# Optimization experiments

Hardware: AMD Instinct MI355X
Metric: run time of the kernel (lower is better)

## Reference

```python
import jax, jax.numpy as jnp
import numpy as np

G = 512            # voxel grid extent per axis
B = 2              # batches
N_PER_BATCH = 20000
EPS = 1e-5
SLOPE = 0.01       # LeakyReLU default negative_slope
OFFS = [(dx, dy, dz) for dx in (-1, 0, 1) for dy in (-1, 0, 1) for dz in (-1, 0, 1)]


def _keys(coords, stride):
    # coords: [N,4] int32 (batch,x,y,z), multiples of stride -> unique int32 key
    Gs = G // stride
    c = coords[:, 1:] // stride
    return ((coords[:, 0] * Gs + c[:, 0]) * Gs + c[:, 1]) * Gs + c[:, 2]


def _sorted_keys(in_coords, in_stride):
    keys = _keys(in_coords, in_stride)
    perm = jnp.argsort(keys)
    return keys[perm], perm


def _query(ks, perm, out_coords, off, in_stride):
    # hash-free kernel-map lookup: binary search of neighbor key in sorted keys
    q = out_coords[:, 1:] + jnp.array(off, jnp.int32) * in_stride
    valid = jnp.all((q >= 0) & (q < G), axis=1)
    qc = jnp.clip(q, 0, G - 1) // in_stride
    Gs = G // in_stride
    qk = ((out_coords[:, 0] * Gs + qc[:, 0]) * Gs + qc[:, 1]) * Gs + qc[:, 2]
    pos = jnp.clip(jnp.searchsorted(ks, qk), 0, ks.shape[0] - 1)
    hit = valid & (ks[pos] == qk)
    return jnp.where(hit, perm[pos], 0), hit


def sparse_conv(feats, in_coords, out_coords, W, in_stride):
    # gather-GEMM-scatter sparse conv, kernel 3^3, W: [27, Cin, Cout]
    ks, perm = _sorted_keys(in_coords, in_stride)
    out = jnp.zeros((out_coords.shape[0], W.shape[-1]), feats.dtype)
    for k, off in enumerate(OFFS):
        idx, hit = _query(ks, perm, out_coords, off, in_stride)
        f = jnp.where(hit[:, None], feats[idx], jnp.zeros((), feats.dtype))
        out = out + f @ W[k]
    return out


def sparse_maxpool(feats, in_coords, out_coords, in_stride):
    ks, perm = _sorted_keys(in_coords, in_stride)
    NEG = jnp.asarray(-3.0e38, feats.dtype)
    out = jnp.full((out_coords.shape[0], feats.shape[1]), NEG, feats.dtype)
    for off in OFFS:
        idx, hit = _query(ks, perm, out_coords, off, in_stride)
        out = jnp.maximum(out, jnp.where(hit[:, None], feats[idx], NEG))
    return out


def slice_to_field(level_feats, level_coords, field_coords, stride):
    # TensorField.slice: map coarse sparse features back to every field point
    ks, perm = _sorted_keys(level_coords, stride)
    qk = _keys(field_coords, stride)
    pos = jnp.clip(jnp.searchsorted(ks, qk), 0, ks.shape[0] - 1)
    return level_feats[perm[pos]]


def bn_lrelu(x, gamma, beta):
    # MinkowskiBatchNorm (training-mode batch stats) + LeakyReLU
    mu = x.mean(0)
    var = ((x - mu) ** 2).mean(0)
    y = (x - mu) * jax.lax.rsqrt(var + EPS) * gamma + beta
    return jnp.where(y >= 0, y, SLOPE * y)


def setup_inputs() -> dict:
    rng = np.random.default_rng(0)
    coords_np = []
    for b in range(B):
        lin = np.unique(rng.integers(0, G ** 3, size=2 * N_PER_BATCH, dtype=np.int64))
        rng.shuffle(lin)
        lin = lin[:N_PER_BATCH]
        x, r = lin // (G * G), lin % (G * G)
        coords_np.append(np.stack([np.full(N_PER_BATCH, b, np.int64), x, r // G, r % G], 1))
    coords_np = np.concatenate(coords_np, 0)

    def level(s):
        q = coords_np.copy()
        q[:, 1:] = (q[:, 1:] // s) * s
        key = ((q[:, 0] * G + q[:, 1]) * G + q[:, 2]) * G + q[:, 3]
        uk = np.unique(key)
        b, r = uk // G ** 3, uk % G ** 3
        return np.stack([b, r // (G * G), (r // G) % G, r % G], 1).astype(np.int32)

    levels = {('c%d' % s): jnp.asarray(level(s)) for s in (2, 4, 8, 16, 32, 64, 128)}
    ks = jax.random.split(jax.random.key(0), 9)

    def conv_w(k, cin, cout):
        return jax.random.normal(k, (27, cin, cout), jnp.float32) * np.float32(np.sqrt(2.0 / (27 * cin)))

    inp = dict(
        feats=jax.random.normal(ks[0], (coords_np.shape[0], 1), jnp.float32),
        coords=jnp.asarray(coords_np.astype(np.int32)),
        w_mlp=jax.random.normal(ks[1], (1, 32), jnp.float32),
        gm=jnp.ones(32, jnp.float32), bm=jnp.zeros(32, jnp.float32),
        W1=conv_w(ks[2], 32, 48), g1=jnp.ones(48, jnp.float32), b1=jnp.zeros(48, jnp.float32),
        W2=conv_w(ks[3], 48, 64), g2=jnp.ones(64, jnp.float32), b2=jnp.zeros(64, jnp.float32),
        W3=conv_w(ks[4], 64, 96), g3=jnp.ones(96, jnp.float32), b3=jnp.zeros(96, jnp.float32),
        W4=conv_w(ks[5], 96, 128), g4=jnp.ones(128, jnp.float32), b4=jnp.zeros(128, jnp.float32),
        W5a=conv_w(ks[6], 336, 256), g5a=jnp.ones(256, jnp.float32), b5a=jnp.zeros(256, jnp.float32),
        W5b=conv_w(ks[7], 256, 512), g5b=jnp.ones(512, jnp.float32), b5b=jnp.zeros(512, jnp.float32),
        W5c=conv_w(ks[8], 512, 1024), g5c=jnp.ones(1024, jnp.float32), b5c=jnp.zeros(1024, jnp.float32),
    )
    inp.update(levels)
    return inp


def reference(feats, coords, c2, c4, c8, c16, c32, c64, c128, w_mlp, gm, bm,
              W1, g1, b1, W2, g2, b2, W3, g3, b3, W4, g4, b4,
              W5a, g5a, b5a, W5b, g5b, b5b, W5c, g5c, b5c):
    # mlp1 on the tensor field (coords are unique, so field == sparse tensor)
    x = bn_lrelu(feats @ w_mlp, gm, bm)                            # [N,32]
    y = bn_lrelu(sparse_conv(x, coords, coords, W1, 1), g1, b1)    # stride 1, 48
    y1 = sparse_maxpool(y, coords, c2, 1)                          # stride 2
    y = bn_lrelu(sparse_conv(y1, c2, c4, W2, 2), g2, b2)           # stride 4, 64
    y2 = sparse_maxpool(y, c4, c8, 4)                              # stride 8
    y = bn_lrelu(sparse_conv(y2, c8, c16, W3, 8), g3, b3)          # stride 16, 96
    y3 = sparse_maxpool(y, c16, c32, 16)                           # stride 32
    y = bn_lrelu(sparse_conv(y3, c32, c64, W4, 32), g4, b4)        # stride 64, 128
    y4 = sparse_maxpool(y, c64, c128, 64)                          # stride 128
    x1 = slice_to_field(y1, c2, coords, 2)
    x2 = slice_to_field(y2, c8, coords, 8)
    x3 = slice_to_field(y3, c32, coords, 32)
    x4 = slice_to_field(y4, c128, coords, 128)
    xc = jnp.concatenate([x1, x2, x3, x4], axis=1)                 # [N,336]
    y = bn_lrelu(sparse_conv(xc, coords, c2, W5a, 1), g5a, b5a)    # stride 2, 256
    y = bn_lrelu(sparse_conv(y, c2, c4, W5b, 2), g5b, b5b)         # stride 4, 512
    y = bn_lrelu(sparse_conv(y, c4, c8, W5c, 4), g5c, b5c)         # stride 8, 1024
    return y
```

## Files before the change

kernel.cpp:

```cpp
#include <hip/hip_runtime.h>
#include <cstdint>
#include <cstddef>

#define GDIM 512

typedef __attribute__((ext_vector_type(8))) short short8;
typedef __attribute__((ext_vector_type(4))) float f32x4;
typedef __attribute__((ext_vector_type(4))) unsigned short ushort4v;

__device__ __forceinline__ short f2bf(float f) {
  unsigned u = __float_as_uint(f);
  u = u + 0x7fffu + ((u >> 16) & 1u);
  return (short)(u >> 16);
}

__device__ __forceinline__ int hash_lookup(int key, const int* __restrict__ keys,
                                           const int* __restrict__ vals, unsigned capmask) {
  unsigned slot = ((unsigned)key * 2654435761u) & capmask;
  while (true) {
    int kk = keys[slot];
    if (kk == key) return vals[slot];
    if (kk == -1) return -1;
    slot = (slot + 1) & capmask;
  }
}

__global__ void k_build_table(const int* __restrict__ coords, int n, int sh, int Gs,
                              int* __restrict__ keys, int* __restrict__ vals, unsigned capmask) {
  int i = blockIdx.x * blockDim.x + threadIdx.x;
  if (i >= n) return;
  int b = coords[4 * i];
  int key = ((b * Gs + (coords[4 * i + 1] >> sh)) * Gs + (coords[4 * i + 2] >> sh)) * Gs +
            (coords[4 * i + 3] >> sh);
  unsigned slot = ((unsigned)key * 2654435761u) & capmask;
  while (true) {
    int prev = atomicCAS(&keys[slot], -1, key);
    if (prev == -1) { vals[slot] = i; return; }
    slot = (slot + 1) & capmask;
  }
}

__global__ void k_query_idx_t(const int* __restrict__ oc, int m, int sh, int Gs,
                              const int* __restrict__ keys, const int* __restrict__ vals,
                              unsigned capmask, int* __restrict__ idxT) {
  int k = blockIdx.y;
  int o = blockIdx.x * blockDim.x + threadIdx.x;
  if (o >= m) return;
  int stride = 1 << sh;
  int dx = k / 9 - 1, dy = (k / 3) % 3 - 1, dz = k % 3 - 1;
  int4 c = *(const int4*)(oc + 4 * o);
  int qx = c.y + dx * stride;
  int qy = c.z + dy * stride;
  int qz = c.w + dz * stride;
  int res = -1;
  if ((unsigned)qx < GDIM && (unsigned)qy < GDIM && (unsigned)qz < GDIM) {
    int key = ((c.x * Gs + (qx >> sh)) * Gs + (qy >> sh)) * Gs + (qz >> sh);
    res = hash_lookup(key, keys, vals, capmask);
  }
  idxT[(size_t)k * m + o] = res;
}

__global__ void k_make_pairs(const int* __restrict__ idxT, int m,
                             int* __restrict__ po_o, int* __restrict__ pi_o,
                             int* __restrict__ po_r, int* __restrict__ pi_r,
                             int* __restrict__ cnts, int mcap) {
  int o = blockIdx.x * blockDim.x + threadIdx.x;
  bool act = o < m;
  int lane = threadIdx.x & 63;
  bool owned = false;
  for (int k = 0; k < 27; ++k) {
    int i = act ? idxT[(size_t)k * m + o] : -1;
    bool hit = i >= 0;
    bool isown = hit && !owned;
    if (isown) owned = true;
    bool isrest = hit && !isown;
    unsigned long long bo = __ballot(isown);
    if (bo) {
      int ldr = __ffsll((unsigned long long)bo) - 1;
      int base = 0;
      if (lane == ldr) base = atomicAdd(&cnts[k], __popcll(bo));
      base = __shfl(base, ldr);
      if (isown) {
        int p = base + __popcll(bo & ((1ull << lane) - 1ull));
        po_o[k * mcap + p] = o;
        pi_o[k * mcap + p] = i;
      }
    }
    unsigned long long br = __ballot(isrest);
    if (br) {
      int ldr = __ffsll((unsigned long long)br) - 1;
      int base = 0;
      if (lane == ldr) base = atomicAdd(&cnts[27 + k], __popcll(br));
      base = __shfl(base, ldr);
      if (isrest) {
        int p = base + __popcll(br & ((1ull << lane) - 1ull));
        po_r[k * mcap + p] = o;
        pi_r[k * mcap + p] = i;
      }
    }
  }
}

template<bool OWNER>
__global__ __launch_bounds__(256) void k_conv_mfma(
    const unsigned short* __restrict__ Fb,
    const short* __restrict__ Wt,
    float* __restrict__ out,
    const int* __restrict__ plo, const int* __restrict__ pli,
    const int* __restrict__ counts, int cin, int cin_pad, int cout, int mcap) {
  int k = blockIdx.z;
  int cnt = counts[k];
  int p0 = blockIdx.x * 64;
  if (p0 >= cnt) return;
  int np = min(64, cnt - p0);

  __shared__ short Alds[64 * 136];
  __shared__ short Blds[2][128 * 40];
  __shared__ int rows_out[64];
  __shared__ int rows_in[64];

  int tid = threadIdx.x;
  if (tid < 64) {
    rows_out[tid] = (tid < np) ? plo[k * mcap + p0 + tid] : -1;
    rows_in [tid] = (tid < np) ? pli[k * mcap + p0 + tid] : -1;
  }

  int wave = tid >> 6, lane = tid & 63;
  int wm = (wave & 1) * 32, wn = (wave >> 1) * 64;
  int lm = lane & 15, quad = lane >> 4;
  const short* Wk = Wt + (size_t)k * cout * cin;
  int nT = (cout + 127) >> 7;
  int nSlab = (cin_pad + 127) >> 7;

  int bn0 = (tid) >> 2, bk0 = (tid & 3) << 3;
  int bn1 = (tid + 256) >> 2, bk1 = ((tid + 256) & 3) << 3;

  for (int nt0 = 0; nt0 < nT; ++nt0) {
    int n0 = nt0 << 7;
    f32x4 acc[2][4] = {};
    for (int ks = 0; ks < cin_pad; ks += 128) {
      int kslab = min(128, cin_pad - ks);
      int aStride = kslab + 8;
      __syncthreads();
      if (nSlab > 1 || nt0 == 0) {
        int clog = kslab == 128 ? 4 : (kslab == 64 ? 3 : 2);
        for (int u = tid; u < (64 << clog); u += 256) {
          int r = u >> clog;
          int kc = (u - (r << clog)) << 3;
          int gk = ks + kc;
          int irow = rows_in[r];
          short8 v = {0, 0, 0, 0, 0, 0, 0, 0};
          if (irow >= 0 && gk < cin)
            v = *(const short8*)((const short*)Fb + (size_t)irow * cin + gk);
          *(short8*)(Alds + r * aStride + kc) = v;
        }
      }
      int nsl = kslab >> 5;
      short8 br0 = {0, 0, 0, 0, 0, 0, 0, 0}, br1 = br0;
      {
        int gn = n0 + bn0, gk = ks + bk0;
        if (gn < cout && gk < cin) br0 = *(const short8*)(Wk + (size_t)gn * cin + gk);
        gn = n0 + bn1; gk = ks + bk1;
        if (gn < cout && gk < cin) br1 = *(const short8*)(Wk + (size_t)gn * cin + gk);
      }
      for (int j = 0; j < nsl; ++j) {
        __syncthreads();
        *(short8*)(&Blds[j & 1][bn0 * 40 + bk0]) = br0;
        *(short8*)(&Blds[j & 1][bn1 * 40 + bk1]) = br1;
        if (j + 1 < nsl) {
          int gkbase = ks + (j + 1) * 32;
          short8 z = {0, 0, 0, 0, 0, 0, 0, 0};
          br0 = z; br1 = z;
          int gn = n0 + bn0, gk = gkbase + bk0;
          if (gn < cout && gk < cin) br0 = *(const short8*)(Wk + (size_t)gn * cin + gk);
          gn = n0 + bn1; gk = gkbase + bk1;
          if (gn < cout && gk < cin) br1 = *(const short8*)(Wk + (size_t)gn * cin + gk);
        }
        __syncthreads();
        int ka = j * 32 + quad * 8;
        short8 a0 = *(const short8*)(Alds + (wm + lm) * aStride + ka);
        short8 a1 = *(const short8*)(Alds + (wm + 16 + lm) * aStride + ka);
        #pragma unroll
        for (int nt = 0; nt < 4; ++nt) {
          short8 b = *(const short8*)(&Blds[j & 1][(wn + nt * 16 + lm) * 40 + quad * 8]);
          acc[0][nt] = __builtin_amdgcn_mfma_f32_16x16x32_bf16(a0, b, acc[0][nt], 0, 0, 0);
          acc[1][nt] = __builtin_amdgcn_mfma_f32_16x16x32_bf16(a1, b, acc[1][nt], 0, 0, 0);
        }
      }
    }
    #pragma unroll
    for (int mt = 0; mt < 2; ++mt)
      #pragma unroll
      for (int nt = 0; nt < 4; ++nt)
        #pragma unroll
        for (int r = 0; r < 4; ++r) {
          int row = wm + mt * 16 + quad * 4 + r;
          int col = n0 + wn + nt * 16 + lm;
          if (row < np && col < cout) {
            if (OWNER)
              out[(size_t)rows_out[row] * cout + col] = acc[mt][nt][r];
            else
              atomicAdd(&out[(size_t)rows_out[row] * cout + col], acc[mt][nt][r]);
          }
        }
  }
}

__global__ void k_convert_w(const float* __restrict__ W, short* __restrict__ Wt,
                            int cin, int cout) {
  __shared__ float tile[32][33];
  int k = blockIdx.z;
  int n0 = blockIdx.x * 32, c0 = blockIdx.y * 32;
  int tx = threadIdx.x & 31, ty = threadIdx.x >> 5;
  const float* Wk = W + (size_t)k * cin * cout;
  for (int i = ty; i < 32; i += 8) {
    int c = c0 + i, n = n0 + tx;
    tile[i][tx] = (c < cin && n < cout) ? Wk[(size_t)c * cout + n] : 0.f;
  }
  __syncthreads();
  short* Wtk = Wt + (size_t)k * cout * cin;
  for (int i = ty; i < 32; i += 8) {
    int n = n0 + i, c = c0 + tx;
    if (n < cout && c < cin) Wtk[(size_t)n * cin + c] = f2bf(tile[tx][i]);
  }
}

__global__ void k_query_idx(const int* __restrict__ oc, int m, int sh, int Gs,
                            const int* __restrict__ keys, const int* __restrict__ vals,
                            unsigned capmask, int* __restrict__ idx) {
  int t = blockIdx.x * blockDim.x + threadIdx.x;
  if (t >= m * 27) return;
  int o = t / 27, k = t - o * 27;
  int stride = 1 << sh;
  int dx = k / 9 - 1, dy = (k / 3) % 3 - 1, dz = k % 3 - 1;
  int b  = oc[4 * o];
  int qx = oc[4 * o + 1] + dx * stride;
  int qy = oc[4 * o + 2] + dy * stride;
  int qz = oc[4 * o + 3] + dz * stride;
  int res = -1;
  if ((unsigned)qx < GDIM && (unsigned)qy < GDIM && (unsigned)qz < GDIM) {
    int key = ((b * Gs + (qx >> sh)) * Gs + (qy >> sh)) * Gs + (qz >> sh);
    res = hash_lookup(key, keys, vals, capmask);
  }
  idx[t] = res;
}

__global__ void k_maxpool_bn(const float* __restrict__ F, unsigned short* __restrict__ out,
                             const int* __restrict__ idx, int m, int C,
                             const float* __restrict__ ab) {
  long long t = (long long)blockIdx.x * blockDim.x + threadIdx.x;
  if (t >= (long long)m * C) return;
  int o = (int)(t / C), c = (int)(t - (long long)o * C);
  float a = ab[c], b = ab[C + c];
  float best = -3e38f;
  #pragma unroll 1
  for (int k = 0; k < 27; ++k) {
    int i = idx[o * 27 + k];
    if (i >= 0) {
      float y = a * F[(size_t)i * C + c] + b;
      y = fmaxf(y, 0.01f * y);
      best = fmaxf(best, y);
    }
  }
  out[t] = (unsigned short)f2bf(best);
}

__global__ void k_slice_idx(const int* __restrict__ coords, int n, int sh, int Gs,
                            const int* __restrict__ keys, const int* __restrict__ vals,
                            unsigned capmask, int* __restrict__ sidx) {
  int i = blockIdx.x * blockDim.x + threadIdx.x;
  if (i >= n) return;
  int b = coords[4 * i];
  int key = ((b * Gs + (coords[4 * i + 1] >> sh)) * Gs + (coords[4 * i + 2] >> sh)) * Gs +
            (coords[4 * i + 3] >> sh);
  int v = hash_lookup(key, keys, vals, capmask);
  sidx[i] = (v < 0) ? 0 : v;
}

__global__ void k_gather_cols16(const unsigned short* __restrict__ src, int C,
                                const int* __restrict__ sidx,
                                unsigned short* __restrict__ dst, int dstC, int colOff, int n) {
  long long t = (long long)blockIdx.x * blockDim.x + threadIdx.x;
  if (t >= (long long)n * C) return;
  int o = (int)(t / C), c = (int)(t - (long long)o * C);
  dst[(size_t)o * dstC + colOff + c] = src[(size_t)sidx[o] * C + c];
}

__global__ void k_mlp(const float* __restrict__ feats, const float* __restrict__ w,
                      float* __restrict__ x, int n) {
  int t = blockIdx.x * blockDim.x + threadIdx.x;
  if (t >= n * 32) return;
  x[t] = feats[t >> 5] * w[t & 31];
}

__global__ void k_bn_stats(const float* __restrict__ x, int m, int C,
                           float* __restrict__ sums) {
  __shared__ float ls[2][256];
  int tid = threadIdx.x;
  int RL = (C >= 256) ? 1 : (256 / C);
  int c, rl;
  bool active;
  if (C >= 256) { c = blockIdx.y * 256 + tid; rl = 0; active = true; }
  else { c = tid % C; rl = tid / C; active = (tid < RL * C); }
  float s = 0.f, s2 = 0.f;
  if (active) {
    int step = gridDim.x * RL;
    for (int r = blockIdx.x * RL + rl; r < m; r += step) {
      float v = x[(size_t)r * C + c];
      s += v; s2 += v * v;
    }
  }
  if (RL == 1) {
    atomicAdd(&sums[c], s);
    atomicAdd(&sums[C + c], s2);
  } else {
    ls[0][tid] = s; ls[1][tid] = s2;
    __syncthreads();
    if (tid < C) {
      for (int j = 1; j < RL; ++j) { s += ls[0][c + j * C]; s2 += ls[1][c + j * C]; }
      atomicAdd(&sums[c], s);
      atomicAdd(&sums[C + c], s2);
    }
  }
}

__global__ void k_bn_finalize(const float* __restrict__ sums, const float* __restrict__ gamma,
                              const float* __restrict__ beta, int C, float inv_m,
                              float* __restrict__ ab) {
  for (int c = threadIdx.x; c < C; c += 256) {
    float mu  = sums[c] * inv_m;
    float var = sums[C + c] * inv_m - mu * mu;
    float a = rsqrtf(var + 1e-5f) * gamma[c];
    ab[c] = a;
    ab[C + c] = beta[c] - mu * a;
  }
}

__global__ void k_bn_bf16(const float* __restrict__ x, unsigned short* __restrict__ xb,
                          long long total4, int C, const float* __restrict__ ab) {
  long long t = (long long)blockIdx.x * blockDim.x + threadIdx.x;
  if (t >= total4) return;
  long long e = t * 4;
  int c = (int)(e % C);
  float4 v = *(const float4*)(x + e);
  ushort4v o;
  float y0 = ab[c] * v.x + ab[C + c];         o.x = (unsigned short)f2bf(fmaxf(y0, 0.01f * y0));
  float y1 = ab[c + 1] * v.y + ab[C + c + 1]; o.y = (unsigned short)f2bf(fmaxf(y1, 0.01f * y1));
  float y2 = ab[c + 2] * v.z + ab[C + c + 2]; o.z = (unsigned short)f2bf(fmaxf(y2, 0.01f * y2));
  float y3 = ab[c + 3] * v.w + ab[C + c + 3]; o.w = (unsigned short)f2bf(fmaxf(y3, 0.01f * y3));
  *(ushort4v*)(xb + e) = o;
}

__global__ void k_bn_apply(float* __restrict__ x, long long total4, int C,
                           const float* __restrict__ ab) {
  long long t = (long long)blockIdx.x * blockDim.x + threadIdx.x;
  if (t >= total4) return;
  long long e = t * 4;
  int c = (int)(e % C);
  float4 v = *(const float4*)(x + e);
  float y0 = ab[c] * v.x + ab[C + c];         v.x = fmaxf(y0, 0.01f * y0);
  float y1 = ab[c + 1] * v.y + ab[C + c + 1]; v.y = fmaxf(y1, 0.01f * y1);
  float y2 = ab[c + 2] * v.z + ab[C + c + 2]; v.z = fmaxf(y2, 0.01f * y2);
  float y3 = ab[c + 3] * v.w + ab[C + c + 3]; v.w = fmaxf(y3, 0.01f * y3);
  *(float4*)(x + e) = v;
}

static inline int cdiv(int a, int b) { return (a + b - 1) / b; }

extern "C" void kernel_launch(void* const* d_in, const int* in_sizes, int n_in,
                              void* d_out, int out_size, void* d_ws, size_t ws_size,
                              hipStream_t stream) {
  (void)n_in; (void)out_size; (void)ws_size;
  const float* feats  = (const float*)d_in[0];
  const int*   coords = (const int*)d_in[1];
  const float* w_mlp = (const float*)d_in[2];
  const float* gm  = (const float*)d_in[3];  const float* bm  = (const float*)d_in[4];
  const float* W1  = (const float*)d_in[5];  const float* g1  = (const float*)d_in[6];  const float* b1  = (const float*)d_in[7];
  const float* W2  = (const float*)d_in[8];  const float* g2  = (const float*)d_in[9];  const float* b2  = (const float*)d_in[10];
  const float* W3  = (const float*)d_in[11]; const float* g3  = (const float*)d_in[12]; const float* b3  = (const float*)d_in[13];
  const float* W4  = (const float*)d_in[14]; const float* g4  = (const float*)d_in[15]; const float* b4  = (const float*)d_in[16];
  const float* W5a = (const float*)d_in[17]; const float* g5a = (const float*)d_in[18]; const float* b5a = (const float*)d_in[19];
  const float* W5b = (const float*)d_in[20]; const float* g5b = (const float*)d_in[21]; const float* b5b = (const float*)d_in[22];
  const float* W5c = (const float*)d_in[23]; const float* g5c = (const float*)d_in[24]; const float* b5c = (const float*)d_in[25];
  const int*   lvl[7];
  for (int i = 0; i < 7; ++i) lvl[i] = (const int*)d_in[26 + i];

  const int N = in_sizes[0];
  int nl[7];
  for (int i = 0; i < 7; ++i) nl[i] = in_sizes[26 + i] / 4;
  const int n2 = nl[0], n4 = nl[1], n8 = nl[2], n16 = nl[3], n32 = nl[4], n64 = nl[5], n128 = nl[6];

  char* ws = (char*)d_ws;
  size_t off = 0;
  auto alloc = [&](size_t bytes) -> char* {
    off = (off + 255) & ~(size_t)255;
    char* p = ws + off;
    off += bytes;
    return p;
  };

  struct Tab { int* keys; int* vals; unsigned mask; int sh; int Gs; int n; const int* src; };
  Tab tab[8];
  const int* tsrc[8] = {coords, lvl[0], lvl[1], lvl[2], lvl[3], lvl[4], lvl[5], lvl[6]};
  int tn[8] = {N, n2, n4, n8, n16, n32, n64, n128};
  for (int i = 0; i < 8; ++i) {
    int cap = 64;
    while (cap < 2 * tn[i]) cap <<= 1;
    tab[i].keys = (int*)alloc((size_t)cap * 4);
    tab[i].vals = (int*)alloc((size_t)cap * 4);
    tab[i].mask = (unsigned)(cap - 1);
    tab[i].sh = i;
    tab[i].Gs = GDIM >> i;
    tab[i].n = tn[i];
    tab[i].src = tsrc[i];
  }

  int* pout   = (int*)alloc((size_t)27 * N * 4);
  int* pin    = (int*)alloc((size_t)27 * N * 4);
  int* pout_r = (int*)alloc((size_t)27 * N * 4);
  int* pin_r  = (int*)alloc((size_t)27 * N * 4);
  int* counts = (int*)alloc(256);
  int* idxbuf = (int*)alloc((size_t)27 * N * 4);
  int* sidx[4];
  for (int i = 0; i < 4; ++i) sidx[i] = (int*)alloc((size_t)N * 4);
  float* bnsum = (float*)alloc(2 * 1024 * 4);
  float* abuf  = (float*)alloc(2 * 1024 * 4);

  auto mxz = [](size_t a, size_t b) { return a > b ? a : b; };
  size_t szA = mxz(mxz((size_t)N * 32, (size_t)n4 * 64), (size_t)n64 * 128) * 4;
  size_t szB = mxz(mxz((size_t)N * 48, (size_t)n16 * 96), (size_t)n2 * 256) * 4;
  float* RA = (float*)alloc(szA);
  float* RB = (float*)alloc(szB);
  float* RG = (float*)alloc((size_t)n4 * 512 * 4);
  unsigned short* xb  = (unsigned short*)alloc((size_t)N * 32 * 2);
  unsigned short* y1b = (unsigned short*)alloc((size_t)n2 * 48 * 2);
  unsigned short* y2b = (unsigned short*)alloc((size_t)n8 * 64 * 2);
  unsigned short* y3b = (unsigned short*)alloc((size_t)n32 * 96 * 2);
  unsigned short* y4b = (unsigned short*)alloc((size_t)n128 * 128 * 2);
  unsigned short* xcb = (unsigned short*)alloc((size_t)N * 336 * 2);
  unsigned short* t5bb = (unsigned short*)alloc((size_t)n4 * 512 * 2);
  short* Wt1  = (short*)alloc((size_t)27 * 32 * 48 * 2);
  short* Wt2  = (short*)alloc((size_t)27 * 48 * 64 * 2);
  short* Wt3  = (short*)alloc((size_t)27 * 64 * 96 * 2);
  short* Wt4  = (short*)alloc((size_t)27 * 96 * 128 * 2);
  short* Wt5a = (short*)alloc((size_t)27 * 336 * 256 * 2);
  short* Wt5b = (short*)alloc((size_t)27 * 256 * 512 * 2);
  short* Wt5c = (short*)alloc((size_t)27 * 512 * 1024 * 2);

  for (int i = 0; i < 8; ++i)
    hipMemsetAsync(tab[i].keys, 0xFF, (size_t)(tab[i].mask + 1) * 4, stream);
  for (int i = 0; i < 8; ++i)
    k_build_table<<<cdiv(tab[i].n, 256), 256, 0, stream>>>(
        tab[i].src, tab[i].n, tab[i].sh, tab[i].Gs, tab[i].keys, tab[i].vals, tab[i].mask);

  auto convW = [&](const float* W, short* Wt, int cin, int cout) {
    dim3 g(cdiv(cout, 32), cdiv(cin, 32), 27);
    k_convert_w<<<g, 256, 0, stream>>>(W, Wt, cin, cout);
  };
  convW(W1, Wt1, 32, 48);     convW(W2, Wt2, 48, 64);
  convW(W3, Wt3, 64, 96);     convW(W4, Wt4, 96, 128);
  convW(W5a, Wt5a, 336, 256); convW(W5b, Wt5b, 256, 512);
  convW(W5c, Wt5c, 512, 1024);

  auto conv = [&](const unsigned short* Fb, const short* Wt, const int* oc, int m,
                  const Tab& t, int cin, int cout, float* out) {
    hipMemsetAsync(counts, 0, 54 * 4, stream);
    dim3 gq(cdiv(m, 256), 27);
    k_query_idx_t<<<gq, 256, 0, stream>>>(oc, m, t.sh, t.Gs, t.keys, t.vals, t.mask, idxbuf);
    k_make_pairs<<<cdiv(m, 256), 256, 0, stream>>>(idxbuf, m, pout, pin, pout_r, pin_r,
                                                   counts, N);
    int cin_pad = cin <= 32 ? 32 : (cin <= 64 ? 64 : ((cin + 127) & ~127));
    dim3 grid(cdiv(m, 64), 1, 27);
    k_conv_mfma<true><<<grid, 256, 0, stream>>>(Fb, Wt, out, pout, pin, counts,
                                                cin, cin_pad, cout, N);
    k_conv_mfma<false><<<grid, 256, 0, stream>>>(Fb, Wt, out, pout_r, pin_r, counts + 27,
                                                 cin, cin_pad, cout, N);
  };
  auto stats = [&](const float* x, int m, int C, const float* gamma, const float* beta) {
    hipMemsetAsync(bnsum, 0, (size_t)2 * C * 4, stream);
    int CG = (C >= 256) ? (C / 256) : 1;
    int RL = (C >= 256) ? 1 : (256 / C);
    int NS = (C >= 256) ? 512 : 256;
    int maxNS = cdiv(m, RL);
    if (NS > maxNS) NS = maxNS < 1 ? 1 : maxNS;
    dim3 g(NS, CG);
    k_bn_stats<<<g, 256, 0, stream>>>(x, m, C, bnsum);
    k_bn_finalize<<<1, 256, 0, stream>>>(bnsum, gamma, beta, C, 1.0f / (float)m, abuf);
  };
  auto pool = [&](const float* F, const int* oc, int m, const Tab& t, int C,
                  unsigned short* out) {
    k_query_idx<<<cdiv(m * 27, 256), 256, 0, stream>>>(
        oc, m, t.sh, t.Gs, t.keys, t.vals, t.mask, idxbuf);
    long long total = (long long)m * C;
    k_maxpool_bn<<<(int)((total + 255) / 256), 256, 0, stream>>>(F, out, idxbuf, m, C, abuf);
  };
  auto cvt = [&](const float* src, unsigned short* dst, long long total, int C) {
    long long t4 = total / 4;
    k_bn_bf16<<<(int)((t4 + 255) / 256), 256, 0, stream>>>(src, dst, t4, C, abuf);
  };

  float* x = RA;
  k_mlp<<<cdiv(N * 32, 256), 256, 0, stream>>>(feats, w_mlp, x, N);
  stats(x, N, 32, gm, bm);
  cvt(x, xb, (long long)N * 32, 32);

  float* t1 = RB;
  conv(xb, Wt1, coords, N, tab[0], 32, 48, t1);
  stats(t1, N, 48, g1, b1);
  pool(t1, lvl[0], n2, tab[0], 48, y1b);

  float* t2 = RA;
  conv(y1b, Wt2, lvl[1], n4, tab[1], 48, 64, t2);
  stats(t2, n4, 64, g2, b2);
  pool(t2, lvl[2], n8, tab[2], 64, y2b);

  float* t3 = RB;
  conv(y2b, Wt3, lvl[3], n16, tab[3], 64, 96, t3);
  stats(t3, n16, 96, g3, b3);
  pool(t3, lvl[4], n32, tab[4], 96, y3b);

  float* t4 = RA;
  conv(y3b, Wt4, lvl[5], n64, tab[5], 96, 128, t4);
  stats(t4, n64, 128, g4, b4);
  pool(t4, lvl[6], n128, tab[6], 128, y4b);

  k_slice_idx<<<cdiv(N, 256), 256, 0, stream>>>(coords, N, tab[1].sh, tab[1].Gs,
                                                tab[1].keys, tab[1].vals, tab[1].mask, sidx[0]);
  k_slice_idx<<<cdiv(N, 256), 256, 0, stream>>>(coords, N, tab[3].sh, tab[3].Gs,
                                                tab[3].keys, tab[3].vals, tab[3].mask, sidx[1]);
  k_slice_idx<<<cdiv(N, 256), 256, 0, stream>>>(coords, N, tab[5].sh, tab[5].Gs,
                                                tab[5].keys, tab[5].vals, tab[5].mask, sidx[2]);
  k_slice_idx<<<cdiv(N, 256), 256, 0, stream>>>(coords, N, tab[7].sh, tab[7].Gs,
                                                tab[7].keys, tab[7].vals, tab[7].mask, sidx[3]);
  k_gather_cols16<<<(int)(((long long)N * 48 + 255) / 256), 256, 0, stream>>>(y1b, 48, sidx[0], xcb, 336, 0, N);
  k_gather_cols16<<<(int)(((long long)N * 64 + 255) / 256), 256, 0, stream>>>(y2b, 64, sidx[1], xcb, 336, 48, N);
  k_gather_cols16<<<(int)(((long long)N * 96 + 255) / 256), 256, 0, stream>>>(y3b, 96, sidx[2], xcb, 336, 112, N);
  k_gather_cols16<<<(int)(((long long)N * 128 + 255) / 256), 256, 0, stream>>>(y4b, 128, sidx[3], xcb, 336, 208, N);

  float* t5a = RB;
  conv(xcb, Wt5a, lvl[0], n2, tab[0], 336, 256, t5a);
  stats(t5a, n2, 256, g5a, b5a);
  unsigned short* t5ab = xcb;
  cvt(t5a, t5ab, (long long)n2 * 256, 256);

  float* t5b = RG;
  conv(t5ab, Wt5b, lvl[1], n4, tab[1], 256, 512, t5b);
  stats(t5b, n4, 512, g5b, b5b);
  cvt(t5b, t5bb, (long long)n4 * 512, 512);

  float* outp = (float*)d_out;
  conv(t5bb, Wt5c, lvl[2], n8, tab[2], 512, 1024, outp);
  stats(outp, n8, 1024, g5c, b5c);
  long long total4 = (long long)n8 * 1024 / 4;
  k_bn_apply<<<(int)((total4 + 255) / 256), 256, 0, stream>>>(outp, total4, 1024, abuf);
}
```

Baseline: 1.960 ms.

## Compact conv grid via per-offset block plan and split output tiles across grid

Adds a tiny planning kernel that prefix-sums the per-offset pair counts into block offsets. The conv kernel then uses a persistent, grid-stride loop over only the non-empty 64-pair tiles instead of launching cdiv(m,64)*27 blocks, most of which exit immediately. Output-column tiles move from an inner loop onto grid.y, which adds parallelism but means the gathered A tile is reloaded once per output tile. It also adds one extra launch and a serial scan per conv.

```diff
diff --git a/kernel.cpp b/kernel.cpp
--- a/kernel.cpp
+++ b/kernel.cpp
@@ -101,59 +101,73 @@
   }
 }
 
+__global__ void k_plan(const int* __restrict__ cnts, int* __restrict__ plan) {
+  if (threadIdx.x == 0) {
+    int acc = 0;
+    for (int k = 0; k < 27; ++k) { plan[k] = acc; acc += (cnts[k] + 63) >> 6; }
+    plan[27] = acc;
+    acc = 0;
+    for (int k = 0; k < 27; ++k) { plan[28 + k] = acc; acc += (cnts[27 + k] + 63) >> 6; }
+    plan[55] = acc;
+  }
+}
+
 template<bool OWNER>
 __global__ __launch_bounds__(256) void k_conv_mfma(
     const unsigned short* __restrict__ Fb,
     const short* __restrict__ Wt,
     float* __restrict__ out,
     const int* __restrict__ plo, const int* __restrict__ pli,
-    const int* __restrict__ counts, int cin, int cin_pad, int cout, int mcap) {
-  int k = blockIdx.z;
-  int cnt = counts[k];
-  int p0 = blockIdx.x * 64;
-  if (p0 >= cnt) return;
-  int np = min(64, cnt - p0);
-
+    const int* __restrict__ counts, const int* __restrict__ plan,
+    int cin, int cin_pad, int cout, int mcap) {
+  __shared__ int pshared[28];
   __shared__ short Alds[64 * 136];
   __shared__ short Blds[2][128 * 40];
   __shared__ int rows_out[64];
   __shared__ int rows_in[64];
 
   int tid = threadIdx.x;
-  if (tid < 64) {
-    rows_out[tid] = (tid < np) ? plo[k * mcap + p0 + tid] : -1;
-    rows_in [tid] = (tid < np) ? pli[k * mcap + p0 + tid] : -1;
-  }
-
+  if (tid < 28) pshared[tid] = plan[tid];
+  __syncthreads();
+  int NB = pshared[27];
+
+  int n0 = blockIdx.y << 7;
   int wave = tid >> 6, lane = tid & 63;
   int wm = (wave & 1) * 32, wn = (wave >> 1) * 64;
   int lm = lane & 15, quad = lane >> 4;
-  const short* Wk = Wt + (size_t)k * cout * cin;
-  int nT = (cout + 127) >> 7;
-  int nSlab = (cin_pad + 127) >> 7;
-
   int bn0 = (tid) >> 2, bk0 = (tid & 3) << 3;
   int bn1 = (tid + 256) >> 2, bk1 = ((tid + 256) & 3) << 3;
 
-  for (int nt0 = 0; nt0 < nT; ++nt0) {
-    int n0 = nt0 << 7;
+  for (int v = blockIdx.x; v < NB; v += gridDim.x) {
+    int k = 0;
+    #pragma unroll
+    for (int kk = 1; kk < 27; ++kk) k += (v >= pshared[kk]);
+    int cnt = counts[k];
+    int p0 = (v - pshared[k]) << 6;
+    int np = min(64, cnt - p0);
+
+    __syncthreads();
+    if (tid < 64) {
+      rows_out[tid] = (tid < np) ? plo[k * mcap + p0 + tid] : -1;
+      rows_in [tid] = (tid < np) ? pli[k * mcap + p0 + tid] : -1;
+    }
+    const short* Wk = Wt + (size_t)k * cout * cin;
     f32x4 acc[2][4] = {};
+
     for (int ks = 0; ks < cin_pad; ks += 128) {
       int kslab = min(128, cin_pad - ks);
       int aStride = kslab + 8;
       __syncthreads();
-      if (nSlab > 1 || nt0 == 0) {
-        int clog = kslab == 128 ? 4 : (kslab == 64 ? 3 : 2);
-        for (int u = tid; u < (64 << clog); u += 256) {
-          int r = u >> clog;
-          int kc = (u - (r << clog)) << 3;
-          int gk = ks + kc;
-          int irow = rows_in[r];
-          short8 v = {0, 0, 0, 0, 0, 0, 0, 0};
-          if (irow >= 0 && gk < cin)
-            v = *(const short8*)((const short*)Fb + (size_t)irow * cin + gk);
-          *(short8*)(Alds + r * aStride + kc) = v;
-        }
+      int clog = kslab == 128 ? 4 : (kslab == 64 ? 3 : 2);
+      for (int u = tid; u < (64 << clog); u += 256) {
+        int r = u >> clog;
+        int kc = (u - (r << clog)) << 3;
+        int gk = ks + kc;
+        int irow = rows_in[r];
+        short8 v8 = {0, 0, 0, 0, 0, 0, 0, 0};
+        if (irow >= 0 && gk < cin)
+          v8 = *(const short8*)((const short*)Fb + (size_t)irow * cin + gk);
+        *(short8*)(Alds + r * aStride + kc) = v8;
       }
       int nsl = kslab >> 5;
       short8 br0 = {0, 0, 0, 0, 0, 0, 0, 0}, br1 = br0;
@@ -420,6 +434,7 @@
   int* pout_r = (int*)alloc((size_t)27 * N * 4);
   int* pin_r  = (int*)alloc((size_t)27 * N * 4);
   int* counts = (int*)alloc(256);
+  int* plan   = (int*)alloc(256);
   int* idxbuf = (int*)alloc((size_t)27 * N * 4);
   int* sidx[4];
   for (int i = 0; i < 4; ++i) sidx[i] = (int*)alloc((size_t)N * 4);
@@ -469,12 +484,16 @@
     k_query_idx_t<<<gq, 256, 0, stream>>>(oc, m, t.sh, t.Gs, t.keys, t.vals, t.mask, idxbuf);
     k_make_pairs<<<cdiv(m, 256), 256, 0, stream>>>(idxbuf, m, pout, pin, pout_r, pin_r,
                                                    counts, N);
+    k_plan<<<1, 64, 0, stream>>>(counts, plan);
     int cin_pad = cin <= 32 ? 32 : (cin <= 64 ? 64 : ((cin + 127) & ~127));
-    dim3 grid(cdiv(m, 64), 1, 27);
-    k_conv_mfma<true><<<grid, 256, 0, stream>>>(Fb, Wt, out, pout, pin, counts,
-                                                cin, cin_pad, cout, N);
-    k_conv_mfma<false><<<grid, 256, 0, stream>>>(Fb, Wt, out, pout_r, pin_r, counts + 27,
+    int nT = cdiv(cout, 128);
+    int G = cdiv(m, 64) + 27;
+    if (G > 2048) G = 2048;
+    dim3 gridc(G, nT);
+    k_conv_mfma<true><<<gridc, 256, 0, stream>>>(Fb, Wt, out, pout, pin, counts, plan,
                                                  cin, cin_pad, cout, N);
+    k_conv_mfma<false><<<gridc, 256, 0, stream>>>(Fb, Wt, out, pout_r, pin_r, counts + 27,
+                                                  plan + 28, cin, cin_pad, cout, N);
   };
   auto stats = [&](const float* x, int m, int C, const float* gamma, const float* beta) {
     hipMemsetAsync(bnsum, 0, (size_t)2 * C * 4, stream);
```

Measured after the change: 1.861 ms. -5.0%, faster.
